# Kernel tuning notes

Hardware: AMD Instinct MI355X
Metric: run time of the kernel (lower is better)

## Reference

```python
import jax, jax.numpy as jnp
import numpy as np

# Sizes
N = 4096        # nodes
E = 32768       # edges
NEF = 128       # n_edge_features
HID = 128       # hidden_features
MUL0 = 64       # multiplicity of 0e irreps
MUL1 = 16       # multiplicity of 1o irreps
DIM = MUL0 + 3 * MUL1  # 112
# e3nn FullyConnectedTensorProduct('64x0e+16x1o', '1x0e+1x1o', '64x0e+16x1o')
# instruction order (i_in1, i_in2, i_out): (0,0,0),(0,1,1),(1,0,1),(1,1,0)
WN_A = MUL0 * MUL0   # 0e x 0e -> 0e : 4096
WN_B = MUL0 * MUL1   # 0e x 1o -> 1o : 1024
WN_C = MUL1 * MUL1   # 1o x 0e -> 1o : 256
WN_D = MUL1 * MUL0   # 1o x 1o -> 0e : 1024
WNUM = WN_A + WN_B + WN_C + WN_D  # 6400
# path normalization (irrep_normalization='component', path_normalization='element'):
# alpha = dim(ir_out) / sum_{paths into same output}(mul1*mul2)
N0 = float(np.sqrt(1.0 / (MUL0 + MUL1)))       # scalar output: 1/sqrt(80)
N1 = float(np.sqrt(3.0 / (MUL0 + MUL1)))       # vector output: sqrt(3/80)
INV_SQRT3 = float(1.0 / np.sqrt(3.0))          # wigner-3j factor for l=1 paths


def setup_inputs() -> dict:
    key = jax.random.key(0)
    ks = jax.random.split(key, 8)
    node_attr = jax.random.normal(ks[0], (N, DIM), jnp.float32)
    edge_index = jax.random.randint(ks[1], (2, E), 0, N)
    edge_attr = jax.random.normal(ks[2], (E, NEF), jnp.float32)
    edge_sh = jax.random.normal(ks[3], (E, 4), jnp.float32)
    global_graph_embedding = jax.random.normal(ks[4], (8, 1024), jnp.float32)
    ptr = jnp.sort(jax.random.randint(ks[5], (9,), 0, N))
    W1 = jax.random.normal(ks[6], (NEF, HID), jnp.float32) / np.sqrt(NEF)
    b1 = jnp.zeros((HID,), jnp.float32)
    W2 = jax.random.normal(ks[7], (HID, WNUM), jnp.float32) / np.sqrt(HID)
    b2 = jnp.zeros((WNUM,), jnp.float32)
    return dict(node_attr=node_attr, edge_index=edge_index, edge_attr=edge_attr,
                edge_sh=edge_sh, global_graph_embedding=global_graph_embedding,
                ptr=ptr, W1=W1, b1=b1, W2=W2, b2=b2)


def _tp_conv(node_attr, src, dst, edge_attr, edge_sh, W1, b1, W2, b2):
    # edge MLP -> per-edge tensor-product weights
    h = jax.nn.relu(edge_attr @ W1 + b1)
    w = h @ W2 + b2                                   # (E, 6400)
    # gather and split gathered node features into irreps
    x = node_attr[dst]                                # (E, 112)
    s = x[:, :MUL0]                                   # (E, 64) scalars 0e
    v = x[:, MUL0:].reshape(-1, MUL1, 3)              # (E, 16, 3) vectors 1o
    sh0 = edge_sh[:, :1]                              # (E, 1)
    sh1 = edge_sh[:, 1:]                              # (E, 3)
    i = 0
    wA = w[:, i:i + WN_A].reshape(-1, MUL0, MUL0); i += WN_A
    wB = w[:, i:i + WN_B].reshape(-1, MUL0, MUL1); i += WN_B
    wC = w[:, i:i + WN_C].reshape(-1, MUL1, MUL1); i += WN_C
    wD = w[:, i:i + WN_D].reshape(-1, MUL1, MUL0); i += WN_D
    # scalar output channel: 0e*0e->0e  and  1o.1o->0e (dot product CG)
    out0 = N0 * (jnp.einsum('euw,eu->ew', wA, s) * sh0
                 + INV_SQRT3 * jnp.einsum('euw,eui,ei->ew', wD, v, sh1))
    # vector output channel: 0e*1o->1o  and  1o*0e->1o
    out1 = N1 * (INV_SQRT3 * jnp.einsum('euw,eu,ei->ewi', wB, s, sh1)
                 + INV_SQRT3 * jnp.einsum('euw,eui->ewi', wC, v) * sh0[:, :, None])
    tp = jnp.concatenate([out0, out1.reshape(-1, 3 * MUL1)], axis=-1)  # (E, 112)
    # scatter-mean over edge_src (torch_scatter 'mean': empty segments -> 0)
    sums = jax.ops.segment_sum(tp, src, num_segments=N)
    cnt = jax.ops.segment_sum(jnp.ones((tp.shape[0],), tp.dtype), src, num_segments=N)
    return sums / jnp.maximum(cnt, 1.0)[:, None]


def reference(node_attr, edge_index, edge_attr, edge_sh, global_graph_embedding, ptr, W1, b1, W2, b2):
    src, dst = edge_index[0], edge_index[1]
    out = _tp_conv(node_attr, src, dst, edge_attr, edge_sh, W1, b1, W2, b2)
    # add_in=False -> global branch skipped; residual: in/out dims equal so F.pad is identity
    return out + node_attr
```

## Files before the change

kernel.cpp:

```cpp
#include <hip/hip_runtime.h>

typedef unsigned short u16;
typedef __bf16 bf8 __attribute__((ext_vector_type(8)));
typedef float f4 __attribute__((ext_vector_type(4)));

#define E_EDGES 32768
#define N_NODES 4096
#define N0_CONST 0.1118033988749895f
#define INV_SQRT3_CONST 0.5773502691896258f

__device__ __forceinline__ u16 f2bf(float f) {
    unsigned u = __float_as_uint(f);
    u += 0x7FFFu + ((u >> 16) & 1u);
    return (u16)(u >> 16);
}

__global__ __launch_bounds__(256) void k_prep(const float* __restrict__ W2, const float* __restrict__ W1,
                                              u16* __restrict__ w2s, u16* __restrict__ w1t,
                                              int* __restrict__ deg, float* __restrict__ outz) {
    int b = blockIdx.x;
    int tid = threadIdx.x;
    if (b < 400) {
        __shared__ float w2l[128][17];
        {
            int k = tid >> 1, c8 = (tid & 1) * 8;
            const float* src = W2 + (size_t)k * 6400 + b * 16 + c8;
            float tmpf[8];
#pragma unroll
            for (int j = 0; j < 8; j++) tmpf[j] = src[j];
#pragma unroll
            for (int j = 0; j < 8; j++) w2l[k][c8 + j] = tmpf[j];
        }
        __syncthreads();
        int ks = tid >> 6, l = tid & 63;
        int el = l & 15, q4 = l >> 4;
        u16 tmp[8];
#pragma unroll
        for (int j = 0; j < 8; j++)
            tmp[j] = f2bf(w2l[ks * 32 + q4 * 8 + j][el]);
        *(uint4*)(w2s + b * 2048 + ks * 512 + l * 8) = *(uint4*)tmp;
    } else if (b < 416) {
        int t = (b - 400) * 256 + tid;
#pragma unroll
        for (int i = 0; i < 4; i++) {
            int idx = t * 4 + i;
            int c = idx >> 7, k = idx & 127;
            w1t[idx] = f2bf(W1[k * 128 + c]);
        }
    } else if (b == 416) {
        *(int4*)&deg[tid * 16] = (int4){0, 0, 0, 0};
        *(int4*)&deg[tid * 16 + 4] = (int4){0, 0, 0, 0};
        *(int4*)&deg[tid * 16 + 8] = (int4){0, 0, 0, 0};
        *(int4*)&deg[tid * 16 + 12] = (int4){0, 0, 0, 0};
    } else {
        float4 z = {0.f, 0.f, 0.f, 0.f};
        float* p = outz + ((size_t)(b - 417) * 256 + tid) * 32;
#pragma unroll
        for (int i = 0; i < 8; i++) *(float4*)(p + i * 4) = z;
    }
}

__global__ __launch_bounds__(256, 2) void k_main(const u16* __restrict__ w2s,
                                                 const u16* __restrict__ w1t,
                                                 const float* __restrict__ b1,
                                                 const float* __restrict__ ea,
                                                 const float* __restrict__ b2,
                                                 const float* __restrict__ node_attr,
                                                 const int* __restrict__ edge_index,
                                                 const float* __restrict__ edge_sh,
                                                 int* __restrict__ deg,
                                                 float* __restrict__ outsum) {
    __shared__ alignas(16) union {
        u16 h[64][136];
        struct { float bcB[64][17]; float bcC[3][64][17]; } bc;
    } ovl;
    __shared__ float sT[64][66];
    __shared__ float vT[3][16][66];
    __shared__ float pT[16][66];
    __shared__ float sh0_s[64];
    __shared__ float sh1_s[3][64];
    __shared__ int dst_s[64];
    __shared__ int src_s[64];

    int tid = threadIdx.x;
    int e0 = blockIdx.x * 64;
    int lane = tid & 63, wave = tid >> 6;
    int el = lane & 15, q4 = lane >> 4;

    bf8 a0[4], a1[4];
    float4 bb0, bb1;
    auto loadA = [&](int i, bf8 (&a)[4], float4& bb) {
        int g = (i < 20) ? 64 + i : (i < 84 ? i - 20 : i);
        int pn = 4 * g + wave;
        const u16* gp = w2s + (size_t)pn * 2048 + lane * 8;
        a[0] = *(const bf8*)(gp);
        a[1] = *(const bf8*)(gp + 512);
        a[2] = *(const bf8*)(gp + 1024);
        a[3] = *(const bf8*)(gp + 1536);
        bb = *(const float4*)(b2 + pn * 16 + q4 * 4);
    };
    loadA(0, a0, bb0);

    if (tid < 64) {
        int ge = e0 + tid;
        int s = edge_index[ge];
        src_s[tid] = s;
        atomicAdd(&deg[s], 1);
        dst_s[tid] = edge_index[E_EDGES + ge];
        float4 sh = *(const float4*)(edge_sh + (size_t)ge * 4);
        sh0_s[tid] = sh.x; sh1_s[0][tid] = sh.y; sh1_s[1][tid] = sh.z; sh1_s[2][tid] = sh.w;
    }
    __syncthreads();

    {
        int e = tid >> 2, q = tid & 3;
        int dst = dst_s[e];
        const float* xp = node_attr + (size_t)dst * 112;
#pragma unroll
        for (int i = 0; i < 4; i++) {
            float4 f = *(const float4*)(xp + q * 16 + i * 4);
            int u = q * 16 + i * 4;
            sT[u + 0][e] = f.x; sT[u + 1][e] = f.y; sT[u + 2][e] = f.z; sT[u + 3][e] = f.w;
        }
        float vv[12];
#pragma unroll
        for (int i = 0; i < 3; i++) {
            float4 f = *(const float4*)(xp + 64 + q * 12 + i * 4);
            vv[i * 4 + 0] = f.x; vv[i * 4 + 1] = f.y; vv[i * 4 + 2] = f.z; vv[i * 4 + 3] = f.w;
        }
        float s1x = sh1_s[0][e], s1y = sh1_s[1][e], s1z = sh1_s[2][e];
#pragma unroll
        for (int u = 0; u < 4; u++) {
            float xa = vv[u * 3 + 0], xb = vv[u * 3 + 1], xc = vv[u * 3 + 2];
            int uu = q * 4 + u;
            vT[0][uu][e] = xa; vT[1][uu][e] = xb; vT[2][uu][e] = xc;
            pT[uu][e] = INV_SQRT3_CONST * (xa * s1x + xb * s1y + xc * s1z);
        }
        const float4* src = (const float4*)(ea + (size_t)(e0 + e) * 128 + q * 32);
#pragma unroll
        for (int i = 0; i < 8; i++) {
            float4 f = src[i];
            int c = q * 32 + i * 4;
            ovl.h[e][c + 0] = f2bf(f.x); ovl.h[e][c + 1] = f2bf(f.y);
            ovl.h[e][c + 2] = f2bf(f.z); ovl.h[e][c + 3] = f2bf(f.w);
        }
    }
    __syncthreads();

    {
        f4 hacc[4][2];
#pragma unroll
        for (int m = 0; m < 4; m++)
#pragma unroll
            for (int nt = 0; nt < 2; nt++) hacc[m][nt] = (f4){0.f, 0.f, 0.f, 0.f};
#pragma unroll
        for (int ks = 0; ks < 4; ks++) {
            bf8 a[4], b[2];
#pragma unroll
            for (int m = 0; m < 4; m++) a[m] = *(const bf8*)&ovl.h[m * 16 + el][ks * 32 + q4 * 8];
#pragma unroll
            for (int nt = 0; nt < 2; nt++) {
                int n = wave * 32 + nt * 16 + el;
                b[nt] = *(const bf8*)(w1t + n * 128 + ks * 32 + q4 * 8);
            }
#pragma unroll
            for (int m = 0; m < 4; m++)
#pragma unroll
                for (int nt = 0; nt < 2; nt++)
                    hacc[m][nt] = __builtin_amdgcn_mfma_f32_16x16x32_bf16(a[m], b[nt], hacc[m][nt], 0, 0, 0);
        }
        __syncthreads();
#pragma unroll
        for (int m = 0; m < 4; m++)
#pragma unroll
            for (int nt = 0; nt < 2; nt++) {
                int n = wave * 32 + nt * 16 + el;
                float bias = b1[n];
#pragma unroll
                for (int r = 0; r < 4; r++) {
                    int e = m * 16 + q4 * 4 + r;
                    ovl.h[e][n] = f2bf(fmaxf(hacc[m][nt][r] + bias, 0.f));
                }
            }
    }
    __syncthreads();

    bf8 hbf[4][4];
#pragma unroll
    for (int nt = 0; nt < 4; nt++)
#pragma unroll
        for (int ks = 0; ks < 4; ks++)
            hbf[nt][ks] = *(const bf8*)&ovl.h[nt * 16 + el][ks * 32 + q4 * 8];
    float sh0n4[4];
#pragma unroll
    for (int nt = 0; nt < 4; nt++) sh0n4[nt] = sh0_s[nt * 16 + el];
    __syncthreads();

    for (int idx = tid; idx < 4352; idx += 256) ((float*)&ovl.bc)[idx] = 0.f;
    __syncthreads();

    auto mfmaG = [&](const bf8 (&a)[4], const float4& bb, f4 (&wf)[4]) {
#pragma unroll
        for (int nt = 0; nt < 4; nt++) wf[nt] = (f4){bb.x, bb.y, bb.z, bb.w};
#pragma unroll
        for (int ks = 0; ks < 4; ks++)
#pragma unroll
            for (int nt = 0; nt < 4; nt++)
                wf[nt] = __builtin_amdgcn_mfma_f32_16x16x32_bf16(a[ks], hbf[nt][ks], wf[nt], 0, 0, 0);
    };

#define STEP(INXT, ACUR, BBCUR, ANXT, BBNXT, CON) \
    { if ((INXT) < 100) loadA((INXT), ANXT, BBNXT); mfmaG(ACUR, BBCUR, wf); CON; }

    f4 wf[4];

    {
        f4 accBn[4];
#pragma unroll
        for (int nt = 0; nt < 4; nt++) accBn[nt] = (f4){0.f, 0.f, 0.f, 0.f};
        auto conB = [&](int ib) {
            int u = 4 * ib + wave;
#pragma unroll
            for (int nt = 0; nt < 4; nt++) {
                float f = sT[u][nt * 16 + el];
                accBn[nt] += f * wf[nt];
            }
        };
        for (int ii = 0; ii < 16; ii += 2) {
            STEP(ii + 1, a0, bb0, a1, bb1, conB(ii));
            STEP(ii + 2, a1, bb1, a0, bb0, conB(ii + 1));
        }
#pragma unroll
        for (int nt = 0; nt < 4; nt++)
#pragma unroll
            for (int r = 0; r < 4; r++)
                atomicAdd(&ovl.bc.bcB[nt * 16 + el][q4 * 4 + r], accBn[nt][r]);
    }

    {
        f4 accCn[3][4];
#pragma unroll
        for (int i3 = 0; i3 < 3; i3++)
#pragma unroll
            for (int nt = 0; nt < 4; nt++) accCn[i3][nt] = (f4){0.f, 0.f, 0.f, 0.f};
        auto conC = [&](int ic) {
            int u = 4 * ic + wave;
#pragma unroll
            for (int nt = 0; nt < 4; nt++) {
#pragma unroll
                for (int i3 = 0; i3 < 3; i3++) {
                    float f = vT[i3][u][nt * 16 + el];
                    accCn[i3][nt] += f * wf[nt];
                }
            }
        };
        for (int ii = 0; ii < 4; ii += 2) {
            STEP(16 + ii + 1, a0, bb0, a1, bb1, conC(ii));
            STEP(16 + ii + 2, a1, bb1, a0, bb0, conC(ii + 1));
        }
#pragma unroll
        for (int i3 = 0; i3 < 3; i3++)
#pragma unroll
            for (int nt = 0; nt < 4; nt++)
#pragma unroll
                for (int r = 0; r < 4; r++)
                    atomicAdd(&ovl.bc.bcC[i3][nt * 16 + el][q4 * 4 + r], accCn[i3][nt][r]);
    }

    f4 acc0n[4];
#pragma unroll
    for (int nt = 0; nt < 4; nt++) acc0n[nt] = (f4){0.f, 0.f, 0.f, 0.f};
    {
        auto conA = [&](int ia) {
#pragma unroll
            for (int nt = 0; nt < 4; nt++) {
                float f = sh0n4[nt] * sT[ia][nt * 16 + el];
                acc0n[nt] += f * wf[nt];
            }
        };
        for (int ii = 0; ii < 64; ii += 2) {
            STEP(20 + ii + 1, a0, bb0, a1, bb1, conA(ii));
            STEP(20 + ii + 2, a1, bb1, a0, bb0, conA(ii + 1));
        }
        auto conD = [&](int id_) {
#pragma unroll
            for (int nt = 0; nt < 4; nt++) {
                float f = pT[id_][nt * 16 + el];
                acc0n[nt] += f * wf[nt];
            }
        };
        for (int ii = 0; ii < 16; ii += 2) {
            STEP(84 + ii + 1, a0, bb0, a1, bb1, conD(ii));
            STEP(84 + ii + 2, a1, bb1, a0, bb0, conD(ii + 1));
        }
    }
#undef STEP

    __syncthreads();

#pragma unroll
    for (int nt = 0; nt < 4; nt++)
#pragma unroll
        for (int r = 0; r < 4; r++)
            sT[nt * 16 + el][wave * 16 + q4 * 4 + r] = N0_CONST * acc0n[nt][r];
    {
        float* vflat = (float*)vT;
        for (int idx = tid; idx < 3072; idx += 256) {
            int e = idx / 48;
            int rem = idx - e * 48;
            int w = rem / 3;
            int i3 = rem - w * 3;
            vflat[idx] = N0_CONST * (ovl.bc.bcB[e][w] * sh1_s[i3][e] + ovl.bc.bcC[i3][e][w] * sh0_s[e]);
        }
    }
    __syncthreads();

    {
        const float* vflat = (const float*)vT;
        for (int idx = tid; idx < 64 * 112; idx += 256) {
            int e = idx / 112;
            int c = idx - e * 112;
            float val = (c < 64) ? sT[e][c] : vflat[e * 48 + (c - 64)];
            atomicAdd(&outsum[(size_t)src_s[e] * 112 + c], val);
        }
    }
}

__global__ __launch_bounds__(128) void k_fin(const int* __restrict__ deg,
                                             const float* __restrict__ node_attr,
                                             float* __restrict__ out) {
    int n = blockIdx.x;
    int c = threadIdx.x;
    if (c >= 112) return;
    float d = fmaxf((float)deg[n], 1.f);
    out[n * 112 + c] = out[n * 112 + c] / d + node_attr[n * 112 + c];
}

extern "C" void kernel_launch(void* const* d_in, const int* in_sizes, int n_in,
                              void* d_out, int out_size, void* d_ws, size_t ws_size,
                              hipStream_t stream) {
    const float* node_attr  = (const float*)d_in[0];
    const int*   edge_index = (const int*)d_in[1];
    const float* edge_attr  = (const float*)d_in[2];
    const float* edge_sh    = (const float*)d_in[3];
    const float* W1         = (const float*)d_in[6];
    const float* b1         = (const float*)d_in[7];
    const float* W2         = (const float*)d_in[8];
    const float* b2         = (const float*)d_in[9];
    float* out = (float*)d_out;

    char* ws = (char*)d_ws;
    u16*   w2s    = (u16*)ws;
    u16*   w1t    = (u16*)(ws + 1638400);
    int*   deg    = (int*)(ws + 1671168);

    k_prep<<<473, 256, 0, stream>>>(W2, W1, w2s, w1t, deg, out);
    k_main<<<512, 256, 0, stream>>>(w2s, w1t, b1, edge_attr, b2, node_attr, edge_index, edge_sh, deg, out);
    k_fin<<<4096, 128, 0, stream>>>(deg, node_attr, out);
}
```

Measured before the change: 180.8 us.

## Fuse prep, main and finalize kernels into one cooperative launch with grid syncs

Merges the three kernel launches into a single cooperative kernel of 512 blocks that does weight conversion and zeroing, grid-syncs, runs the main edge body, grid-syncs again, and then applies the mean-normalization plus residual in a grid-stride loop. The aim is to remove launch overhead and inter-kernel gaps. In exchange it adds two grid-wide barriers, raises shared memory use because the prep staging buffer is now resident alongside the main body's buffers, which may limit occupancy, and needs all 512 blocks co-resident. If the cooperative launch fails it falls back to the original three launches.

```diff
diff --git a/kernel.cpp b/kernel.cpp
--- a/kernel.cpp
+++ b/kernel.cpp
@@ -1,4 +1,7 @@
 #include <hip/hip_runtime.h>
+#include <hip/hip_cooperative_groups.h>
+
+namespace cg = cooperative_groups;
 
 typedef unsigned short u16;
 typedef __bf16 bf8 __attribute__((ext_vector_type(8)));
@@ -14,6 +17,7 @@
     u += 0x7FFFu + ((u >> 16) & 1u);
     return (u16)(u >> 16);
 }
+
 
 __global__ __launch_bounds__(256) void k_prep(const float* __restrict__ W2, const float* __restrict__ W1,
                                               u16* __restrict__ w2s, u16* __restrict__ w1t,
@@ -60,16 +64,17 @@
     }
 }
 
-__global__ __launch_bounds__(256, 2) void k_main(const u16* __restrict__ w2s,
-                                                 const u16* __restrict__ w1t,
-                                                 const float* __restrict__ b1,
-                                                 const float* __restrict__ ea,
-                                                 const float* __restrict__ b2,
-                                                 const float* __restrict__ node_attr,
-                                                 const int* __restrict__ edge_index,
-                                                 const float* __restrict__ edge_sh,
-                                                 int* __restrict__ deg,
-                                                 float* __restrict__ outsum) {
+__device__ __forceinline__ void main_body(int b, int tid,
+                                          const u16* __restrict__ w2s,
+                                          const u16* __restrict__ w1t,
+                                          const float* __restrict__ b1,
+                                          const float* __restrict__ ea,
+                                          const float* __restrict__ b2,
+                                          const float* __restrict__ node_attr,
+                                          const int* __restrict__ edge_index,
+                                          const float* __restrict__ edge_sh,
+                                          int* __restrict__ deg,
+                                          float* __restrict__ outsum) {
     __shared__ alignas(16) union {
         u16 h[64][136];
         struct { float bcB[64][17]; float bcC[3][64][17]; } bc;
@@ -82,8 +87,7 @@
     __shared__ int dst_s[64];
     __shared__ int src_s[64];
 
-    int tid = threadIdx.x;
-    int e0 = blockIdx.x * 64;
+    int e0 = b * 64;
     int lane = tid & 63, wave = tid >> 6;
     int el = lane & 15, q4 = lane >> 4;
 
@@ -155,19 +159,19 @@
             for (int nt = 0; nt < 2; nt++) hacc[m][nt] = (f4){0.f, 0.f, 0.f, 0.f};
 #pragma unroll
         for (int ks = 0; ks < 4; ks++) {
-            bf8 a[4], b[2];
+            bf8 a[4], bb[2];
 #pragma unroll
             for (int m = 0; m < 4; m++) a[m] = *(const bf8*)&ovl.h[m * 16 + el][ks * 32 + q4 * 8];
 #pragma unroll
             for (int nt = 0; nt < 2; nt++) {
                 int n = wave * 32 + nt * 16 + el;
-                b[nt] = *(const bf8*)(w1t + n * 128 + ks * 32 + q4 * 8);
+                bb[nt] = *(const bf8*)(w1t + n * 128 + ks * 32 + q4 * 8);
             }
 #pragma unroll
             for (int m = 0; m < 4; m++)
 #pragma unroll
                 for (int nt = 0; nt < 2; nt++)
-                    hacc[m][nt] = __builtin_amdgcn_mfma_f32_16x16x32_bf16(a[m], b[nt], hacc[m][nt], 0, 0, 0);
+                    hacc[m][nt] = __builtin_amdgcn_mfma_f32_16x16x32_bf16(a[m], bb[nt], hacc[m][nt], 0, 0, 0);
         }
         __syncthreads();
 #pragma unroll
@@ -324,6 +328,19 @@
             atomicAdd(&outsum[(size_t)src_s[e] * 112 + c], val);
         }
     }
+}
+
+__global__ __launch_bounds__(256, 2) void k_main(const u16* __restrict__ w2s,
+                                                 const u16* __restrict__ w1t,
+                                                 const float* __restrict__ b1,
+                                                 const float* __restrict__ ea,
+                                                 const float* __restrict__ b2,
+                                                 const float* __restrict__ node_attr,
+                                                 const int* __restrict__ edge_index,
+                                                 const float* __restrict__ edge_sh,
+                                                 int* __restrict__ deg,
+                                                 float* __restrict__ outsum) {
+    main_body(blockIdx.x, threadIdx.x, w2s, w1t, b1, ea, b2, node_attr, edge_index, edge_sh, deg, outsum);
 }
 
 __global__ __launch_bounds__(128) void k_fin(const int* __restrict__ deg,
@@ -334,6 +351,78 @@
     if (c >= 112) return;
     float d = fmaxf((float)deg[n], 1.f);
     out[n * 112 + c] = out[n * 112 + c] / d + node_attr[n * 112 + c];
+}
+
+__global__ __launch_bounds__(256, 2) void k_all(const float* __restrict__ W2,
+                                                const float* __restrict__ W1,
+                                                const float* __restrict__ b1,
+                                                const float* __restrict__ ea,
+                                                const float* __restrict__ b2,
+                                                const float* __restrict__ node_attr,
+                                                const int* __restrict__ edge_index,
+                                                const float* __restrict__ edge_sh,
+                                                u16* __restrict__ w2s,
+                                                u16* __restrict__ w1t,
+                                                int* __restrict__ deg,
+                                                float* __restrict__ outsum) {
+    cg::grid_group grid = cg::this_grid();
+    int tid = threadIdx.x;
+    int b = blockIdx.x;
+
+    if (b < 400) {
+        __shared__ float w2l[128][17];
+        {
+            int k = tid >> 1, c8 = (tid & 1) * 8;
+            const float* src = W2 + (size_t)k * 6400 + b * 16 + c8;
+            float tmpf[8];
+#pragma unroll
+            for (int j = 0; j < 8; j++) tmpf[j] = src[j];
+#pragma unroll
+            for (int j = 0; j < 8; j++) w2l[k][c8 + j] = tmpf[j];
+        }
+        __syncthreads();
+        int ks = tid >> 6, l = tid & 63;
+        int el = l & 15, q4 = l >> 4;
+        u16 tmp[8];
+#pragma unroll
+        for (int j = 0; j < 8; j++)
+            tmp[j] = f2bf(w2l[ks * 32 + q4 * 8 + j][el]);
+        *(uint4*)(w2s + b * 2048 + ks * 512 + l * 8) = *(uint4*)tmp;
+        __syncthreads();
+    } else if (b < 416) {
+        int t = (b - 400) * 256 + tid;
+#pragma unroll
+        for (int i = 0; i < 4; i++) {
+            int idx = t * 4 + i;
+            int c = idx >> 7, k = idx & 127;
+            w1t[idx] = f2bf(W1[k * 128 + c]);
+        }
+    } else if (b == 416) {
+        *(int4*)&deg[tid * 16] = (int4){0, 0, 0, 0};
+        *(int4*)&deg[tid * 16 + 4] = (int4){0, 0, 0, 0};
+        *(int4*)&deg[tid * 16 + 8] = (int4){0, 0, 0, 0};
+        *(int4*)&deg[tid * 16 + 12] = (int4){0, 0, 0, 0};
+    } else if (b < 473) {
+        float4 z = {0.f, 0.f, 0.f, 0.f};
+        float* p = outsum + ((size_t)(b - 417) * 256 + tid) * 32;
+#pragma unroll
+        for (int i = 0; i < 8; i++) *(float4*)(p + i * 4) = z;
+    }
+    __threadfence();
+    grid.sync();
+
+    main_body(b, tid, w2s, w1t, b1, ea, b2, node_attr, edge_index, edge_sh, deg, outsum);
+
+    __threadfence();
+    grid.sync();
+    {
+        int gtid = b * 256 + tid;
+        for (int idx = gtid; idx < N_NODES * 112; idx += 512 * 256) {
+            int n = idx / 112;
+            float d = fmaxf((float)deg[n], 1.f);
+            outsum[idx] = outsum[idx] / d + node_attr[idx];
+        }
+    }
 }
 
 extern "C" void kernel_launch(void* const* d_in, const int* in_sizes, int n_in,
@@ -354,7 +443,14 @@
     u16*   w1t    = (u16*)(ws + 1638400);
     int*   deg    = (int*)(ws + 1671168);
 
-    k_prep<<<473, 256, 0, stream>>>(W2, W1, w2s, w1t, deg, out);
-    k_main<<<512, 256, 0, stream>>>(w2s, w1t, b1, edge_attr, b2, node_attr, edge_index, edge_sh, deg, out);
-    k_fin<<<4096, 128, 0, stream>>>(deg, node_attr, out);
-}
+    void* args[] = {(void*)&W2, (void*)&W1, (void*)&b1, (void*)&edge_attr, (void*)&b2,
+                    (void*)&node_attr, (void*)&edge_index, (void*)&edge_sh,
+                    (void*)&w2s, (void*)&w1t, (void*)&deg, (void*)&out};
+    hipError_t err = hipLaunchCooperativeKernel((void*)k_all, dim3(512), dim3(256), args, 0, stream);
+    if (err != hipSuccess) {
+        (void)hipGetLastError();
+        k_prep<<<473, 256, 0, stream>>>(W2, W1, w2s, w1t, deg, out);
+        k_main<<<512, 256, 0, stream>>>(w2s, w1t, b1, edge_attr, b2, node_attr, edge_index, edge_sh, deg, out);
+        k_fin<<<4096, 128, 0, stream>>>(deg, node_attr, out);
+    }
+}
```

Measured after the change: 409.4 us. 126% more time.

## Fuse finalize pass into main kernel via grid-wide atomic barrier

Applied to the files above, without the earlier changes.

Removes the separate k_fin launch. After its scatter atomics, each k_main block joins a software grid barrier: a counter that k_prep zeroes, bumped with atomicAdd and spin-waited with acquire loads. All blocks then cooperatively apply the mean division and residual add. This saves one kernel launch and its gap, but it relies on all 512 blocks being co-resident (launch bounds 256,2 on 256 CUs); otherwise the kernel deadlocks. The spin-wait also adds tail latency.

```diff
diff --git a/kernel.cpp b/kernel.cpp
--- a/kernel.cpp
+++ b/kernel.cpp
@@ -17,7 +17,8 @@
 
 __global__ __launch_bounds__(256) void k_prep(const float* __restrict__ W2, const float* __restrict__ W1,
                                               u16* __restrict__ w2s, u16* __restrict__ w1t,
-                                              int* __restrict__ deg, float* __restrict__ outz) {
+                                              int* __restrict__ deg, int* __restrict__ bar,
+                                              float* __restrict__ outz) {
     int b = blockIdx.x;
     int tid = threadIdx.x;
     if (b < 400) {
@@ -52,6 +53,7 @@
         *(int4*)&deg[tid * 16 + 4] = (int4){0, 0, 0, 0};
         *(int4*)&deg[tid * 16 + 8] = (int4){0, 0, 0, 0};
         *(int4*)&deg[tid * 16 + 12] = (int4){0, 0, 0, 0};
+        if (tid == 0) *bar = 0;
     } else {
         float4 z = {0.f, 0.f, 0.f, 0.f};
         float* p = outz + ((size_t)(b - 417) * 256 + tid) * 32;
@@ -69,6 +71,7 @@
                                                  const int* __restrict__ edge_index,
                                                  const float* __restrict__ edge_sh,
                                                  int* __restrict__ deg,
+                                                 int* __restrict__ bar,
                                                  float* __restrict__ outsum) {
     __shared__ alignas(16) union {
         u16 h[64][136];
@@ -83,7 +86,8 @@
     __shared__ int src_s[64];
 
     int tid = threadIdx.x;
-    int e0 = blockIdx.x * 64;
+    int b = blockIdx.x;
+    int e0 = b * 64;
     int lane = tid & 63, wave = tid >> 6;
     int el = lane & 15, q4 = lane >> 4;
 
@@ -155,19 +159,19 @@
             for (int nt = 0; nt < 2; nt++) hacc[m][nt] = (f4){0.f, 0.f, 0.f, 0.f};
 #pragma unroll
         for (int ks = 0; ks < 4; ks++) {
-            bf8 a[4], b[2];
+            bf8 a[4], bb[2];
 #pragma unroll
             for (int m = 0; m < 4; m++) a[m] = *(const bf8*)&ovl.h[m * 16 + el][ks * 32 + q4 * 8];
 #pragma unroll
             for (int nt = 0; nt < 2; nt++) {
                 int n = wave * 32 + nt * 16 + el;
-                b[nt] = *(const bf8*)(w1t + n * 128 + ks * 32 + q4 * 8);
+                bb[nt] = *(const bf8*)(w1t + n * 128 + ks * 32 + q4 * 8);
             }
 #pragma unroll
             for (int m = 0; m < 4; m++)
 #pragma unroll
                 for (int nt = 0; nt < 2; nt++)
-                    hacc[m][nt] = __builtin_amdgcn_mfma_f32_16x16x32_bf16(a[m], b[nt], hacc[m][nt], 0, 0, 0);
+                    hacc[m][nt] = __builtin_amdgcn_mfma_f32_16x16x32_bf16(a[m], bb[nt], hacc[m][nt], 0, 0, 0);
         }
         __syncthreads();
 #pragma unroll
@@ -324,16 +328,24 @@
             atomicAdd(&outsum[(size_t)src_s[e] * 112 + c], val);
         }
     }
-}
-
-__global__ __launch_bounds__(128) void k_fin(const int* __restrict__ deg,
-                                             const float* __restrict__ node_attr,
-                                             float* __restrict__ out) {
-    int n = blockIdx.x;
-    int c = threadIdx.x;
-    if (c >= 112) return;
-    float d = fmaxf((float)deg[n], 1.f);
-    out[n * 112 + c] = out[n * 112 + c] / d + node_attr[n * 112 + c];
+
+    __threadfence();
+    __syncthreads();
+    if (tid == 0) {
+        atomicAdd(bar, 1);
+        while (__hip_atomic_load(bar, __ATOMIC_ACQUIRE, __HIP_MEMORY_SCOPE_AGENT) < 512) {}
+    }
+    __syncthreads();
+    __threadfence();
+
+    {
+        int gtid = b * 256 + tid;
+        for (int idx = gtid; idx < N_NODES * 112; idx += 512 * 256) {
+            int n = idx / 112;
+            float d = fmaxf((float)deg[n], 1.f);
+            outsum[idx] = outsum[idx] / d + node_attr[idx];
+        }
+    }
 }
 
 extern "C" void kernel_launch(void* const* d_in, const int* in_sizes, int n_in,
@@ -353,8 +365,8 @@
     u16*   w2s    = (u16*)ws;
     u16*   w1t    = (u16*)(ws + 1638400);
     int*   deg    = (int*)(ws + 1671168);
-
-    k_prep<<<473, 256, 0, stream>>>(W2, W1, w2s, w1t, deg, out);
-    k_main<<<512, 256, 0, stream>>>(w2s, w1t, b1, edge_attr, b2, node_attr, edge_index, edge_sh, deg, out);
-    k_fin<<<4096, 128, 0, stream>>>(deg, node_attr, out);
+    int*   bar    = (int*)(ws + 1687552);
+
+    k_prep<<<473, 256, 0, stream>>>(W2, W1, w2s, w1t, deg, bar, out);
+    k_main<<<512, 256, 0, stream>>>(w2s, w1t, b1, edge_attr, b2, node_attr, edge_index, edge_sh, deg, bar, out);
 }
```

After: 329.8 us. 82.4% more time.
